# Performance work log

Measured on AMD Instinct MI355X. Metric: run time of the kernel, lower is better.

Reference implementation:

```python
import jax, jax.numpy as jnp
import numpy as np

COUPLE_STRENGTH = 0.1
ITER_FISTA = 16
ITER_EIGENVAL = 20


def setup_inputs() -> dict:
    key = jax.random.key(0)
    k1, k2 = jax.random.split(key)
    # light field patches: (b, N, u, v, s, t, ch)
    x = jax.random.normal(k1, (8, 256, 5, 5, 4, 4, 3), dtype=jnp.float32)
    dim_signal = 5 * 5 * 4 * 4 * 3  # 1200
    dim_dict = 2 * dim_signal       # overcompleteness = 2 -> 2400
    D = jax.random.normal(k2, (dim_signal, dim_dict), dtype=jnp.float32)
    D = D / jnp.linalg.norm(D, axis=0, keepdims=True)  # UnitNorm(axis=0) constraint
    return {"x": x, "dictionary": D}


def _max_eigval(D):
    """von Mises power iteration for largest eigenvalue of D^T D."""
    v0 = jax.random.normal(jax.random.key(42), (D.shape[1],), dtype=D.dtype)
    v0 = v0 / jnp.linalg.norm(v0)

    def step(v, _):
        w = D.T @ (D @ v)
        n = jnp.linalg.norm(w)
        return w / n, n

    _, norms = jax.lax.scan(step, v0, None, length=ITER_EIGENVAL)
    return norms[-1]


def _soft_threshold(x, thr):
    return jnp.sign(x) * jnp.maximum(jnp.abs(x) - thr, 0.0)


def _sparse_code_fista(x2, D):
    """x2: (B, N, dim_signal); D: (dim_signal, dim_dict) -> codes (B, N, dim_dict)."""
    L = _max_eigval(D)            # Lipschitz constant of grad of 0.5*||Dz - x||^2
    thr = COUPLE_STRENGTH / L
    z0 = jnp.zeros(x2.shape[:-1] + (D.shape[1],), dtype=x2.dtype)
    carry0 = (z0, z0, jnp.float32(1.0))  # (z, y, t)

    def step(carry, _):
        z, y, t = carry
        recon = jnp.einsum('bnk,dk->bnd', y, D)             # (B,N,ds)
        grad = jnp.einsum('bnd,dk->bnk', recon - x2, D)     # (B,N,dd)
        z_new = _soft_threshold(y - grad / L, thr)
        t_new = 0.5 * (1.0 + jnp.sqrt(1.0 + 4.0 * t * t))
        y_new = z_new + ((t - 1.0) / t_new) * (z_new - z)   # Nesterov momentum
        return (z_new, y_new, t_new), None

    (z, _, _), _ = jax.lax.scan(step, carry0, None, length=ITER_FISTA)
    return z


def reference(x, dictionary):
    B, N, u, v, s, t, ch = x.shape
    x2 = x.reshape(B, N, u * v * s * t * ch)
    code = jax.lax.stop_gradient(_sparse_code_fista(x2, dictionary))
    recon = jnp.einsum('bnk,dk->bnd', code, dictionary)  # matmul(x, D, transpose_b=True)
    return recon.reshape(B, N, u, v, s, t, ch)
```

## Files before the change

### kernel.cpp

```cpp
#include <hip/hip_runtime.h>
#include <hip/hip_bf16.h>
#include <cmath>

#define DS 1200
#define DD 2400
#define MR 2048
#define KP 1216
#define NP1 1280
#define NG 2432
#define PPI 150

typedef __attribute__((ext_vector_type(8))) short s16x8;
typedef __attribute__((ext_vector_type(4))) float f32x4;

__device__ __forceinline__ float s2f(short s) {
    union { unsigned u; float f; } c;
    c.u = ((unsigned)(unsigned short)s) << 16;
    return c.f;
}
__device__ __forceinline__ short f2s(float f) {
    __hip_bfloat16 h = __float2bfloat16(f);
    return *reinterpret_cast<short*>(&h);
}


__device__ __forceinline__ unsigned rotl32(unsigned x, int d) {
    return (x << d) | (x >> (32 - d));
}

__device__ void threefry2x32(unsigned k0, unsigned k1, unsigned x0, unsigned x1,
                             unsigned* o0, unsigned* o1) {
    unsigned ks0 = k0, ks1 = k1, ks2 = k0 ^ k1 ^ 0x1BD11BDAu;
    const int rotA[4] = {13, 15, 26, 6};
    const int rotB[4] = {17, 29, 16, 24};
    x0 += ks0; x1 += ks1;
    #pragma unroll
    for (int r = 0; r < 4; r++) { x0 += x1; x1 = rotl32(x1, rotA[r]); x1 ^= x0; }
    x0 += ks1; x1 += ks2 + 1u;
    #pragma unroll
    for (int r = 0; r < 4; r++) { x0 += x1; x1 = rotl32(x1, rotB[r]); x1 ^= x0; }
    x0 += ks2; x1 += ks0 + 2u;
    #pragma unroll
    for (int r = 0; r < 4; r++) { x0 += x1; x1 = rotl32(x1, rotA[r]); x1 ^= x0; }
    x0 += ks0; x1 += ks1 + 3u;
    #pragma unroll
    for (int r = 0; r < 4; r++) { x0 += x1; x1 = rotl32(x1, rotB[r]); x1 ^= x0; }
    x0 += ks1; x1 += ks2 + 4u;
    #pragma unroll
    for (int r = 0; r < 4; r++) { x0 += x1; x1 = rotl32(x1, rotA[r]); x1 ^= x0; }
    x0 += ks2; x1 += ks0 + 5u;
    *o0 = x0; *o1 = x1;
}

__device__ float erfinv_f32(float x) {
    float w = -logf((1.0f - x) * (1.0f + x));
    float p;
    if (w < 5.0f) {
        w -= 2.5f;
        p = 2.81022636e-08f;
        p = fmaf(p, w, 3.43273939e-07f);
        p = fmaf(p, w, -3.5233877e-06f);
        p = fmaf(p, w, -4.39150654e-06f);
        p = fmaf(p, w, 0.00021858087f);
        p = fmaf(p, w, -0.00125372503f);
        p = fmaf(p, w, -0.00417768164f);
        p = fmaf(p, w, 0.246640727f);
        p = fmaf(p, w, 1.50140941f);
    } else {
        w = sqrtf(w) - 3.0f;
        p = -0.000200214257f;
        p = fmaf(p, w, 0.000100950558f);
        p = fmaf(p, w, 0.00134934322f);
        p = fmaf(p, w, -0.00367342844f);
        p = fmaf(p, w, 0.00573950773f);
        p = fmaf(p, w, -0.0076224613f);
        p = fmaf(p, w, 0.00943887047f);
        p = fmaf(p, w, 1.00167406f);
        p = fmaf(p, w, 2.83297682f);
    }
    return p * x;
}

__device__ float bits_to_normal(unsigned bits) {
    unsigned fb = (bits >> 9) | 0x3F800000u;
    float u01 = __uint_as_float(fb) - 1.0f;
    const float lo = -0.99999994f;
    float u = u01 * 2.0f + lo;
    u = fmaxf(lo, u);
    return 1.41421356237f * erfinv_f32(u);
}

__global__ void k_init(float* __restrict__ w0, float* __restrict__ w1,
                       float* __restrict__ part) {
    int tid = threadIdx.x;
    for (int i = tid; i < 21 * PPI; i += 256) part[i] = 0.0f;
    if (tid < 32) {
        w0[2400 + tid] = 0.0f;
        w1[2400 + tid] = 0.0f;
    }
    __shared__ float red[256];
    float local2 = 0.0f;
    for (int p = tid; p < DS; p += 256) {
        unsigned r0, r1;
        threefry2x32(0u, 42u, (unsigned)p, (unsigned)(DS + p), &r0, &r1);
        float n0 = bits_to_normal(r0);
        float n1 = bits_to_normal(r1);
        w0[p] = n0;
        w0[DS + p] = n1;
        local2 += n0 * n0 + n1 * n1;
    }
    red[tid] = local2;
    __syncthreads();
    for (int s = 128; s > 0; s >>= 1) {
        if (tid < s) red[tid] += red[tid + s];
        __syncthreads();
    }
    if (tid == 0) part[0] = red[0];
}

__global__ __launch_bounds__(1024) void k_gmv(const short* __restrict__ Grm,
                                              const float* __restrict__ win,
                                              const float* __restrict__ partin,
                                              float* __restrict__ wout,
                                              float* __restrict__ partout) {
    float s2 = 0.0f;
    for (int i = 0; i < PPI; i++) s2 += partin[i];
    float rn = 1.0f / sqrtf(s2);
    int wave = threadIdx.x >> 6, lane = threadIdx.x & 63;
    int row = blockIdx.x * 16 + wave;
    const s16x8* gh = (const s16x8*)(Grm + (size_t)row * NG);
    const float4* w4 = (const float4*)win;
    float acc = 0.0f;
    #pragma unroll
    for (int i = 0; i < 5; i++) {
        int c = lane + i * 64;
        if (c < 304) {
            s16x8 h = gh[c];
            float4 wa = w4[c * 2], wb = w4[c * 2 + 1];
            acc += s2f(h[0]) * wa.x + s2f(h[1]) * wa.y;
            acc += s2f(h[2]) * wa.z + s2f(h[3]) * wa.w;
            acc += s2f(h[4]) * wb.x + s2f(h[5]) * wb.y;
            acc += s2f(h[6]) * wb.z + s2f(h[7]) * wb.w;
        }
    }
    #pragma unroll
    for (int off = 32; off > 0; off >>= 1) acc += __shfl_xor(acc, off, 64);
    __shared__ float red[16];
    if (lane == 0) {
        float val = acc * rn;
        wout[row] = val;
        red[wave] = val * val;
    }
    __syncthreads();
    if (threadIdx.x == 0) {
        float s = 0.0f;
        #pragma unroll
        for (int i = 0; i < 16; i++) s += red[i];
        partout[blockIdx.x] = s;
    }
}

__global__ void k_fin(const float* __restrict__ part20, float* __restrict__ scal) {
    if (threadIdx.x == 0) {
        float s = 0.0f;
        for (int i = 0; i < PPI; i++) s += part20[i];
        float L = sqrtf(s);
        scal[0] = L;
        scal[1] = 1.0f / L;
        scal[2] = 0.1f / L;
    }
}

__global__ void k_makeD(const float* __restrict__ D, short* __restrict__ Dp) {
    int p = blockIdx.x * 256 + threadIdx.x;
    if (p >= NP1 * NG) return;
    int tile = p >> 10, win = p & 1023;
    int row = win >> 3, e = win & 7;
    int mt = tile / (NG >> 3), ct = tile % (NG >> 3);
    int d = mt * 128 + row, n = ct * 8 + e;
    float v = (d < DS && n < DD) ? D[(size_t)d * DD + n] : 0.0f;
    Dp[p] = f2s(v);
}

__global__ void k_makeX(const float* __restrict__ x,
                        short* __restrict__ Xhi, short* __restrict__ Xlo) {
    int p = blockIdx.x * 256 + threadIdx.x;
    if (p >= MR * KP) return;
    int tile = p >> 10, win = p & 1023;
    int row = win >> 3, e = win & 7;
    int mt = tile / (KP >> 3), ct = tile % (KP >> 3);
    int m = mt * 128 + row, k = ct * 8 + e;
    float v = (k < DS) ? x[(size_t)m * DS + k] : 0.0f;
    short h = f2s(v);
    Xhi[p] = h;
    Xlo[p] = f2s(v - s2f(h));
}

__global__ void k_makeDt(const float* __restrict__ D,
                         short* __restrict__ Dthi, short* __restrict__ Dtlo) {
    __shared__ float t[32][33];
    int bc = blockIdx.x * 32;
    int bk = blockIdx.y * 32;
    int tx = threadIdx.x & 31, ty = threadIdx.x >> 5;
    for (int i = ty; i < 32; i += 8) {
        int k = bk + i, c = bc + tx;
        t[i][tx] = (k < DS && c < DD) ? D[(size_t)k * DD + c] : 0.0f;
    }
    __syncthreads();
    for (int i = ty; i < 32; i += 8) {
        int c = bc + i, k = bk + tx;
        float v = t[tx][i];
        short h = f2s(v);
        size_t po = ((size_t)(c >> 7) * (KP >> 3) + (k >> 3)) * 1024 +
                    ((c & 127) << 3) + (k & 7);
        Dthi[po] = h;
        Dtlo[po] = f2s(v - s2f(h));
    }
}

__global__ void k_makeW(const float* __restrict__ Gf, const float* __restrict__ scal,
                        short* __restrict__ Wp) {
    int i = blockIdx.x * 256 + threadIdx.x;
    if (i >= NG * NG / 8) return;
    float invL = scal[1];
    int e0 = i * 8;
    int band = e0 / (128 * NG);
    int rem = e0 - band * (128 * NG);
    int tile = rem >> 10;
    int row = (rem & 1023) >> 3;
    int m = band * 128 + row;
    int k0 = tile * 8;
    const float4* gp = (const float4*)(Gf + (size_t)m * NG + k0);
    float4 g0 = gp[0], g1 = gp[1];
    float gv[8] = {g0.x, g0.y, g0.z, g0.w, g1.x, g1.y, g1.z, g1.w};
    s16x8 wv;
    #pragma unroll
    for (int e = 0; e < 8; e++) {
        float wf = ((k0 + e == m) ? 1.0f : 0.0f) - gv[e] * invL;
        wv[e] = f2s(wf);
    }
    ((s16x8*)Wp)[i] = wv;
}

__global__ void k_fista0(const short* __restrict__ XDL, const float* __restrict__ scal,
                         short* __restrict__ Z, short* __restrict__ Y) {
    int i = blockIdx.x * 256 + threadIdx.x;
    if (i >= MR * NG / 8) return;
    float thr = scal[2];
    s16x8 xv = ((const s16x8*)XDL)[i];
    s16x8 zs;
    #pragma unroll
    for (int k = 0; k < 8; k++) {
        float gs = s2f(xv[k]);
        float az = fabsf(gs) - thr;
        float zn = (az > 0.0f) ? copysignf(az, gs) : 0.0f;
        zs[k] = f2s(zn);
    }
    ((s16x8*)Z)[i] = zs;
    ((s16x8*)Y)[i] = zs;
}

__device__ __forceinline__ void gload16(const void* g, void* l) {
    __builtin_amdgcn_global_load_lds(
        (const __attribute__((address_space(1))) unsigned int*)g,
        (__attribute__((address_space(3))) unsigned int*)l, 16, 0, 0);
}

template <int EPI, bool SPLIT>
__global__ __launch_bounds__(256, 2) void mfma_gemm(
    const short* __restrict__ Ah, const short* __restrict__ Al, int CA,
    const short* __restrict__ Bh, const short* __restrict__ Bl, int CB,
    int K, int swz,
    const short* __restrict__ XDLp, const float* __restrict__ scal, float mom,
    short* __restrict__ Ynew, short* __restrict__ Zst,
    short* __restrict__ Grm,
    float* __restrict__ Out) {
    constexpr int ALO = 2048;
    constexpr int BHO = 4096;
    constexpr int BLO = 8192;
    constexpr int BUF = 12288;
    __shared__ __align__(16) short lds[3 * BUF];

    const int tid = threadIdx.x;
    const int w = tid >> 6, lane = tid & 63;
    const int fm = lane & 15, kg = lane >> 4;
    const int wr = w >> 1, wc = w & 1;

    int bx, by;
    if (swz) {
        int q = gridDim.x >> 3;
        int s = (blockIdx.x & 7) * q + (blockIdx.x >> 3);
        by = s & 31; bx = s >> 5;
    } else { bx = blockIdx.x; by = blockIdx.y; }
    const int m0 = by * 64, n0 = bx * 128;

    f32x4 acc[2][4];
    #pragma unroll
    for (int g = 0; g < 2; ++g)
        #pragma unroll
        for (int h = 0; h < 4; ++h) acc[g][h] = f32x4{0.f, 0.f, 0.f, 0.f};

    float invL = 0.0f, thr = 0.0f;
    if (EPI == 2) thr = scal[2];
    if (EPI == 3) invL = scal[1];

    const int half = (m0 >> 6) & 1;
    const int nk = K / (SPLIT ? 32 : 64);

    const size_t AbS = (size_t)(m0 & ~127) * CA + w * 1024 + half * 512 + lane * 8;
    const size_t BbS = (size_t)n0 * CB + w * 512 + lane * 8;
    const size_t AbN = (size_t)(m0 & ~127) * CA + half * 512 + lane * 8;
    const size_t BbN = (size_t)n0 * CB + lane * 8;

    auto STAGE = [&](int t, int cur) {
        short* bp = &lds[cur * BUF];
        if constexpr (SPLIT) {
            const size_t kk = (size_t)t << 12;
            gload16(Ah + AbS + kk, bp + w * 512);
            gload16(Bh + BbS + kk, bp + BHO + w * 512);
            gload16(Bh + BbS + kk + 2048, bp + BHO + 2048 + w * 512);
            gload16(Al + AbS + kk, bp + ALO + w * 512);
            gload16(Bl + BbS + kk, bp + BLO + w * 512);
            gload16(Bl + BbS + kk + 2048, bp + BLO + 2048 + w * 512);
        } else {
            const size_t kk = (size_t)t << 13;
            const int cs0 = 2 * w, cs1 = 2 * w + 1;
            gload16(Ah + AbN + kk + cs0 * 1024, bp + cs0 * 512);
            gload16(Ah + AbN + kk + cs1 * 1024, bp + cs1 * 512);
            gload16(Bh + BbN + kk + cs0 * 1024,       bp + BHO + cs0 * 1024);
            gload16(Bh + BbN + kk + cs0 * 1024 + 512, bp + BHO + cs0 * 1024 + 512);
            gload16(Bh + BbN + kk + cs1 * 1024,       bp + BHO + cs1 * 1024);
            gload16(Bh + BbN + kk + cs1 * 1024 + 512, bp + BHO + cs1 * 1024 + 512);
        }
    };

    STAGE(0, 0);
    STAGE(1, 1);

    int rb = 0, sb = 2;
    for (int t = 0; t < nk; ++t) {
        if (t < nk - 1)
            asm volatile("s_waitcnt vmcnt(6)" ::: "memory");
        else
            asm volatile("s_waitcnt vmcnt(0)" ::: "memory");
        __builtin_amdgcn_s_barrier();
        asm volatile("" ::: "memory");
        if (t + 2 < nk) STAGE(t + 2, sb);
        const short* bs = &lds[rb * BUF];

        #pragma unroll
        for (int ks = 0; ks < (SPLIT ? 1 : 2); ++ks) {
            const int c = ks * 4 + kg;
            s16x8 a[2], b[4];
            #pragma unroll
            for (int g = 0; g < 2; ++g)
                a[g] = *(const s16x8*)&bs[c * 512 + (wr * 32 + g * 16 + fm) * 8];
            #pragma unroll
            for (int h = 0; h < 4; ++h)
                b[h] = *(const s16x8*)&bs[BHO + c * 1024 + (wc * 64 + h * 16 + fm) * 8];
            if constexpr (SPLIT) {
                s16x8 a2[2], b2[4];
                #pragma unroll
                for (int g = 0; g < 2; ++g)
                    a2[g] = *(const s16x8*)&bs[ALO + c * 512 + (wr * 32 + g * 16 + fm) * 8];
                #pragma unroll
                for (int h = 0; h < 4; ++h)
                    b2[h] = *(const s16x8*)&bs[BLO + c * 1024 + (wc * 64 + h * 16 + fm) * 8];
                #pragma unroll
                for (int g = 0; g < 2; ++g)
                    #pragma unroll
                    for (int h = 0; h < 4; ++h) {
                        acc[g][h] = __builtin_amdgcn_mfma_f32_16x16x32_bf16(a[g], b[h], acc[g][h], 0, 0, 0);
                        acc[g][h] = __builtin_amdgcn_mfma_f32_16x16x32_bf16(a[g], b2[h], acc[g][h], 0, 0, 0);
                        acc[g][h] = __builtin_amdgcn_mfma_f32_16x16x32_bf16(a2[g], b[h], acc[g][h], 0, 0, 0);
                    }
            } else {
                #pragma unroll
                for (int g = 0; g < 2; ++g)
                    #pragma unroll
                    for (int h = 0; h < 4; ++h)
                        acc[g][h] = __builtin_amdgcn_mfma_f32_16x16x32_bf16(a[g], b[h], acc[g][h], 0, 0, 0);
            }
        }
        rb = (rb == 2) ? 0 : rb + 1;
        sb = (sb == 2) ? 0 : sb + 1;
    }

    #pragma unroll
    for (int g = 0; g < 2; ++g) {
        #pragma unroll
        for (int h = 0; h < 4; ++h) {
            #pragma unroll
            for (int j = 0; j < 4; ++j) {
                int m = m0 + wr * 32 + g * 16 + kg * 4 + j;
                int n = n0 + wc * 64 + h * 16 + fm;
                float v = acc[g][h][j];
                if (EPI == 0) {
                    if (n < DS) Out[(size_t)m * DS + n] = v;
                } else if (EPI == 2) {
                    size_t pz = (size_t)(m & ~127) * NG + ((n >> 3) << 10) +
                                ((m & 127) << 3) + (n & 7);
                    float gs = v + s2f(XDLp[pz]);
                    float az = fabsf(gs) - thr;
                    float zn = (az > 0.0f) ? copysignf(az, gs) : 0.0f;
                    float zold = s2f(Zst[pz]);
                    float yn = zn + mom * (zn - zold);
                    Zst[pz] = f2s(zn);
                    Ynew[pz] = f2s(yn);
                } else if (EPI == 3) {
                    size_t pz = (size_t)(m & ~127) * NG + ((n >> 3) << 10) +
                                ((m & 127) << 3) + (n & 7);
                    Ynew[pz] = f2s(v * invL);
                } else {
                    size_t o = (size_t)m * NG + n;
                    Grm[o] = f2s(v);
                    Out[o] = v;
                }
            }
        }
    }
}

extern "C" void kernel_launch(void* const* d_in, const int* in_sizes, int n_in,
                              void* d_out, int out_size, void* d_ws, size_t ws_size,
                              hipStream_t stream) {
    const float* x = (const float*)d_in[0];
    const float* D = (const float*)d_in[1];
    float* out = (float*)d_out;

    char* wsb = (char*)d_ws;
    float* w0 = (float*)wsb;
    float* w1 = w0 + 2432;
    float* part = w1 + 2432;
    float* scal = part + 3200;

    char* p = wsb + 65536;
    short* Dp   = (short*)p; p += (size_t)NP1 * NG * 2;
    short* Dthi = (short*)p; p += (size_t)NG * KP * 2;
    short* Dtlo = (short*)p; p += (size_t)NG * KP * 2;
    short* Xhi  = (short*)p; p += (size_t)MR * KP * 2;
    short* Xlo  = (short*)p; p += (size_t)MR * KP * 2;
    short* Wp   = (short*)p; p += (size_t)NG * NG * 2;
    short* Grm  = (short*)p; p += (size_t)NG * NG * 2;
    short* XDLp = (short*)p; p += (size_t)MR * NG * 2;
    short* Ya   = (short*)p; p += (size_t)MR * NG * 2;
    short* Yb   = (short*)p; p += (size_t)MR * NG * 2;
    short* Zp   = (short*)p; p += (size_t)MR * NG * 2;
    float* Gf   = (float*)Ya;

    k_makeD<<<(NP1 * NG + 255) / 256, 256, 0, stream>>>(D, Dp);
    k_makeDt<<<dim3(NG / 32, KP / 32), 256, 0, stream>>>(D, Dthi, Dtlo);
    k_makeX<<<(MR * KP + 255) / 256, 256, 0, stream>>>(x, Xhi, Xlo);

    mfma_gemm<4, true><<<dim3(NG / 128, NG / 64), 256, 0, stream>>>(
        Dthi, Dtlo, KP, Dthi, Dtlo, KP, KP, 0,
        nullptr, nullptr, 0.0f, nullptr, nullptr, Grm, Gf);

    k_init<<<1, 256, 0, stream>>>(w0, w1, part);
    for (int j = 0; j < 20; j++) {
        const float* win = (j & 1) ? w1 : w0;
        float* wout = (j & 1) ? w0 : w1;
        k_gmv<<<PPI, 1024, 0, stream>>>(Grm, win, part + j * PPI, wout,
                                        part + (j + 1) * PPI);
    }
    k_fin<<<1, 64, 0, stream>>>(part + 20 * PPI, scal);

    k_makeW<<<(NG * NG / 8 + 255) / 256, 256, 0, stream>>>(Gf, scal, Wp);

    mfma_gemm<3, true><<<dim3(608), 256, 0, stream>>>(
        Xhi, Xlo, KP, Dthi, Dtlo, KP, KP, 1,
        nullptr, scal, 0.0f, XDLp, nullptr, nullptr, nullptr);

    k_fista0<<<(MR * NG / 8 + 255) / 256, 256, 0, stream>>>(XDLp, scal, Zp, Ya);

    float t = 1.6180339887f;
    for (int i = 1; i < 16; i++) {
        float tn = 0.5f * (1.0f + sqrtf(1.0f + 4.0f * t * t));
        float mom = (t - 1.0f) / tn;
        t = tn;
        short* Yc = (i & 1) ? Ya : Yb;
        short* Yn = (i & 1) ? Yb : Ya;
        mfma_gemm<2, false><<<dim3(608), 256, 0, stream>>>(
            Yc, nullptr, NG, Wp, nullptr, NG, NG, 1,
            XDLp, scal, mom, Yn, Zp, nullptr, nullptr);
    }

    mfma_gemm<0, false><<<dim3(320), 256, 0, stream>>>(
        Zp, nullptr, NG, Dp, nullptr, NG, NG, 1,
        nullptr, nullptr, 0.0f, nullptr, nullptr, nullptr, out);
}
```

Measured before the change: 1.002 ms.

## Fuse power iteration into cooperative kernel, shrink GEMM pipeline for occupancy

Replaces the 20 per-iteration matvec launches plus the finalize kernel with a single cooperative kernel that loops over iterations using grid-wide syncs. It stops writing the fp32 Gram copy, so makeW reads the bf16 Gram, which lowers precision of W slightly. The GEMM goes from a three-buffer LDS pipeline with manual waitcnt to two buffers with __syncthreads, and launch bounds are raised to 4 blocks per CU to increase occupancy. The risk is less latency hiding in the GEMM's main loop, plus grid.sync overhead.

```diff
diff --git a/kernel.cpp b/kernel.cpp
--- a/kernel.cpp
+++ b/kernel.cpp
@@ -1,6 +1,9 @@
 #include <hip/hip_runtime.h>
 #include <hip/hip_bf16.h>
+#include <hip/hip_cooperative_groups.h>
 #include <cmath>
+
+namespace cg = cooperative_groups;
 
 #define DS 1200
 #define DD 2400
@@ -8,7 +11,7 @@
 #define KP 1216
 #define NP1 1280
 #define NG 2432
-#define PPI 150
+#define PB 152
 
 typedef __attribute__((ext_vector_type(8))) short s16x8;
 typedef __attribute__((ext_vector_type(4))) float f32x4;
@@ -93,7 +96,7 @@
 __global__ void k_init(float* __restrict__ w0, float* __restrict__ w1,
                        float* __restrict__ part) {
     int tid = threadIdx.x;
-    for (int i = tid; i < 21 * PPI; i += 256) part[i] = 0.0f;
+    for (int i = tid; i < 21 * PB; i += 256) part[i] = 0.0f;
     if (tid < 32) {
         w0[2400 + tid] = 0.0f;
         w1[2400 + tid] = 0.0f;
@@ -118,52 +121,62 @@
     if (tid == 0) part[0] = red[0];
 }
 
-__global__ __launch_bounds__(1024) void k_gmv(const short* __restrict__ Grm,
-                                              const float* __restrict__ win,
-                                              const float* __restrict__ partin,
-                                              float* __restrict__ wout,
-                                              float* __restrict__ partout) {
-    float s2 = 0.0f;
-    for (int i = 0; i < PPI; i++) s2 += partin[i];
-    float rn = 1.0f / sqrtf(s2);
-    int wave = threadIdx.x >> 6, lane = threadIdx.x & 63;
-    int row = blockIdx.x * 16 + wave;
+__global__ __launch_bounds__(1024) void k_power(const short* __restrict__ Grm,
+                                                float* __restrict__ w0,
+                                                float* __restrict__ w1,
+                                                float* __restrict__ part,
+                                                float* __restrict__ scal) {
+    cg::grid_group grid = cg::this_grid();
+    const int wv = threadIdx.x >> 6, lane = threadIdx.x & 63;
+    const int row = blockIdx.x * 16 + wv;
+    __shared__ float red[16];
+    __shared__ float rns;
+
     const s16x8* gh = (const s16x8*)(Grm + (size_t)row * NG);
-    const float4* w4 = (const float4*)win;
-    float acc = 0.0f;
-    #pragma unroll
-    for (int i = 0; i < 5; i++) {
-        int c = lane + i * 64;
-        if (c < 304) {
-            s16x8 h = gh[c];
-            float4 wa = w4[c * 2], wb = w4[c * 2 + 1];
-            acc += s2f(h[0]) * wa.x + s2f(h[1]) * wa.y;
-            acc += s2f(h[2]) * wa.z + s2f(h[3]) * wa.w;
-            acc += s2f(h[4]) * wb.x + s2f(h[5]) * wb.y;
-            acc += s2f(h[6]) * wb.z + s2f(h[7]) * wb.w;
-        }
-    }
-    #pragma unroll
-    for (int off = 32; off > 0; off >>= 1) acc += __shfl_xor(acc, off, 64);
-    __shared__ float red[16];
-    if (lane == 0) {
-        float val = acc * rn;
-        wout[row] = val;
-        red[wave] = val * val;
-    }
-    __syncthreads();
-    if (threadIdx.x == 0) {
+
+    for (int j = 0; j < 20; ++j) {
+        const float* win = (j & 1) ? w1 : w0;
+        float* wout = (j & 1) ? w0 : w1;
+        if (threadIdx.x == 0) {
+            float s = 0.0f;
+            for (int b = 0; b < PB; ++b) s += part[j * PB + b];
+            rns = 1.0f / sqrtf(s);
+        }
+        __syncthreads();
+        const float rn = rns;
+        const float4* w4 = (const float4*)win;
+        float acc = 0.0f;
+        #pragma unroll
+        for (int i = 0; i < 5; i++) {
+            int c = lane + i * 64;
+            if (c < 304) {
+                s16x8 h = gh[c];
+                float4 wa = w4[c * 2], wb = w4[c * 2 + 1];
+                acc += s2f(h[0]) * wa.x + s2f(h[1]) * wa.y;
+                acc += s2f(h[2]) * wa.z + s2f(h[3]) * wa.w;
+                acc += s2f(h[4]) * wb.x + s2f(h[5]) * wb.y;
+                acc += s2f(h[6]) * wb.z + s2f(h[7]) * wb.w;
+            }
+        }
+        #pragma unroll
+        for (int off = 32; off > 0; off >>= 1) acc += __shfl_xor(acc, off, 64);
+        if (lane == 0) {
+            float val = acc * rn;
+            wout[row] = val;
+            red[wv] = val * val;
+        }
+        __syncthreads();
+        if (threadIdx.x == 0) {
+            float s = 0.0f;
+            #pragma unroll
+            for (int i = 0; i < 16; i++) s += red[i];
+            part[(j + 1) * PB + blockIdx.x] = s;
+        }
+        grid.sync();
+    }
+    if (blockIdx.x == 0 && threadIdx.x == 0) {
         float s = 0.0f;
-        #pragma unroll
-        for (int i = 0; i < 16; i++) s += red[i];
-        partout[blockIdx.x] = s;
-    }
-}
-
-__global__ void k_fin(const float* __restrict__ part20, float* __restrict__ scal) {
-    if (threadIdx.x == 0) {
-        float s = 0.0f;
-        for (int i = 0; i < PPI; i++) s += part20[i];
+        for (int b = 0; b < PB; ++b) s += part[20 * PB + b];
         float L = sqrtf(s);
         scal[0] = L;
         scal[1] = 1.0f / L;
@@ -218,7 +231,7 @@
     }
 }
 
-__global__ void k_makeW(const float* __restrict__ Gf, const float* __restrict__ scal,
+__global__ void k_makeW(const short* __restrict__ Grm, const float* __restrict__ scal,
                         short* __restrict__ Wp) {
     int i = blockIdx.x * 256 + threadIdx.x;
     if (i >= NG * NG / 8) return;
@@ -230,13 +243,11 @@
     int row = (rem & 1023) >> 3;
     int m = band * 128 + row;
     int k0 = tile * 8;
-    const float4* gp = (const float4*)(Gf + (size_t)m * NG + k0);
-    float4 g0 = gp[0], g1 = gp[1];
-    float gv[8] = {g0.x, g0.y, g0.z, g0.w, g1.x, g1.y, g1.z, g1.w};
+    s16x8 g = *(const s16x8*)(Grm + (size_t)m * NG + k0);
     s16x8 wv;
     #pragma unroll
     for (int e = 0; e < 8; e++) {
-        float wf = ((k0 + e == m) ? 1.0f : 0.0f) - gv[e] * invL;
+        float wf = ((k0 + e == m) ? 1.0f : 0.0f) - s2f(g[e]) * invL;
         wv[e] = f2s(wf);
     }
     ((s16x8*)Wp)[i] = wv;
@@ -267,7 +278,7 @@
 }
 
 template <int EPI, bool SPLIT>
-__global__ __launch_bounds__(256, 2) void mfma_gemm(
+__global__ __launch_bounds__(256, 4) void mfma_gemm(
     const short* __restrict__ Ah, const short* __restrict__ Al, int CA,
     const short* __restrict__ Bh, const short* __restrict__ Bl, int CB,
     int K, int swz,
@@ -279,7 +290,7 @@
     constexpr int BHO = 4096;
     constexpr int BLO = 8192;
     constexpr int BUF = 12288;
-    __shared__ __align__(16) short lds[3 * BUF];
+    __shared__ __align__(16) short lds[2 * BUF];
 
     const int tid = threadIdx.x;
     const int w = tid >> 6, lane = tid & 63;
@@ -335,18 +346,11 @@
     };
 
     STAGE(0, 0);
-    STAGE(1, 1);
-
-    int rb = 0, sb = 2;
+
     for (int t = 0; t < nk; ++t) {
-        if (t < nk - 1)
-            asm volatile("s_waitcnt vmcnt(6)" ::: "memory");
-        else
-            asm volatile("s_waitcnt vmcnt(0)" ::: "memory");
-        __builtin_amdgcn_s_barrier();
-        asm volatile("" ::: "memory");
-        if (t + 2 < nk) STAGE(t + 2, sb);
-        const short* bs = &lds[rb * BUF];
+        __syncthreads();
+        if (t + 1 < nk) STAGE(t + 1, (t + 1) & 1);
+        const short* bs = &lds[(t & 1) * BUF];
 
         #pragma unroll
         for (int ks = 0; ks < (SPLIT ? 1 : 2); ++ks) {
@@ -382,8 +386,6 @@
                         acc[g][h] = __builtin_amdgcn_mfma_f32_16x16x32_bf16(a[g], b[h], acc[g][h], 0, 0, 0);
             }
         }
-        rb = (rb == 2) ? 0 : rb + 1;
-        sb = (sb == 2) ? 0 : sb + 1;
     }
 
     #pragma unroll
@@ -412,9 +414,7 @@
                                 ((m & 127) << 3) + (n & 7);
                     Ynew[pz] = f2s(v * invL);
                 } else {
-                    size_t o = (size_t)m * NG + n;
-                    Grm[o] = f2s(v);
-                    Out[o] = v;
+                    Grm[(size_t)m * NG + n] = f2s(v);
                 }
             }
         }
@@ -446,7 +446,6 @@
     short* Ya   = (short*)p; p += (size_t)MR * NG * 2;
     short* Yb   = (short*)p; p += (size_t)MR * NG * 2;
     short* Zp   = (short*)p; p += (size_t)MR * NG * 2;
-    float* Gf   = (float*)Ya;
 
     k_makeD<<<(NP1 * NG + 255) / 256, 256, 0, stream>>>(D, Dp);
     k_makeDt<<<dim3(NG / 32, KP / 32), 256, 0, stream>>>(D, Dthi, Dtlo);
@@ -454,18 +453,17 @@
 
     mfma_gemm<4, true><<<dim3(NG / 128, NG / 64), 256, 0, stream>>>(
         Dthi, Dtlo, KP, Dthi, Dtlo, KP, KP, 0,
-        nullptr, nullptr, 0.0f, nullptr, nullptr, Grm, Gf);
+        nullptr, nullptr, 0.0f, nullptr, nullptr, Grm, nullptr);
 
     k_init<<<1, 256, 0, stream>>>(w0, w1, part);
-    for (int j = 0; j < 20; j++) {
-        const float* win = (j & 1) ? w1 : w0;
-        float* wout = (j & 1) ? w0 : w1;
-        k_gmv<<<PPI, 1024, 0, stream>>>(Grm, win, part + j * PPI, wout,
-                                        part + (j + 1) * PPI);
-    }
-    k_fin<<<1, 64, 0, stream>>>(part + 20 * PPI, scal);
-
-    k_makeW<<<(NG * NG / 8 + 255) / 256, 256, 0, stream>>>(Gf, scal, Wp);
+    {
+        void* kargs[] = {(void*)&Grm, (void*)&w0, (void*)&w1,
+                         (void*)&part, (void*)&scal};
+        hipLaunchCooperativeKernel((void*)k_power, dim3(PB), dim3(1024),
+                                   kargs, 0, stream);
+    }
+
+    k_makeW<<<(NG * NG / 8 + 255) / 256, 256, 0, stream>>>(Grm, scal, Wp);
 
     mfma_gemm<3, true><<<dim3(608), 256, 0, stream>>>(
         Xhi, Xlo, KP, Dthi, Dtlo, KP, KP, 1,
```

After: 1.185 ms. 18.2% more time.

## Double-buffer GEMM for higher occupancy, drop X low split, specialize last FISTA step

Applied to the files above, without the earlier changes.

The GEMM pipeline shrinks from a triple-buffered LDS ring with vmcnt waits to double buffering with __syncthreads, and launch bounds rise to four blocks per SM to gain occupancy. The X·D GEMM drops the X low-part split (new SPLITM=2 mode, two MFMAs instead of three). The fp32 Gram output is removed, so W is built from the bf16 Gram. The final FISTA iteration uses a new epilogue that writes only Z and skips the Y update. These changes reduce memory traffic and MFMA work but lower precision and shorten the prefetch distance.

```diff
diff --git a/kernel.cpp b/kernel.cpp
--- a/kernel.cpp
+++ b/kernel.cpp
@@ -182,8 +182,7 @@
     Dp[p] = f2s(v);
 }
 
-__global__ void k_makeX(const float* __restrict__ x,
-                        short* __restrict__ Xhi, short* __restrict__ Xlo) {
+__global__ void k_makeX(const float* __restrict__ x, short* __restrict__ Xp) {
     int p = blockIdx.x * 256 + threadIdx.x;
     if (p >= MR * KP) return;
     int tile = p >> 10, win = p & 1023;
@@ -191,9 +190,7 @@
     int mt = tile / (KP >> 3), ct = tile % (KP >> 3);
     int m = mt * 128 + row, k = ct * 8 + e;
     float v = (k < DS) ? x[(size_t)m * DS + k] : 0.0f;
-    short h = f2s(v);
-    Xhi[p] = h;
-    Xlo[p] = f2s(v - s2f(h));
+    Xp[p] = f2s(v);
 }
 
 __global__ void k_makeDt(const float* __restrict__ D,
@@ -218,7 +215,7 @@
     }
 }
 
-__global__ void k_makeW(const float* __restrict__ Gf, const float* __restrict__ scal,
+__global__ void k_makeW(const short* __restrict__ Grm, const float* __restrict__ scal,
                         short* __restrict__ Wp) {
     int i = blockIdx.x * 256 + threadIdx.x;
     if (i >= NG * NG / 8) return;
@@ -230,13 +227,11 @@
     int row = (rem & 1023) >> 3;
     int m = band * 128 + row;
     int k0 = tile * 8;
-    const float4* gp = (const float4*)(Gf + (size_t)m * NG + k0);
-    float4 g0 = gp[0], g1 = gp[1];
-    float gv[8] = {g0.x, g0.y, g0.z, g0.w, g1.x, g1.y, g1.z, g1.w};
+    s16x8 g = *(const s16x8*)(Grm + (size_t)m * NG + k0);
     s16x8 wv;
     #pragma unroll
     for (int e = 0; e < 8; e++) {
-        float wf = ((k0 + e == m) ? 1.0f : 0.0f) - gv[e] * invL;
+        float wf = ((k0 + e == m) ? 1.0f : 0.0f) - s2f(g[e]) * invL;
         wv[e] = f2s(wf);
     }
     ((s16x8*)Wp)[i] = wv;
@@ -266,8 +261,8 @@
         (__attribute__((address_space(3))) unsigned int*)l, 16, 0, 0);
 }
 
-template <int EPI, bool SPLIT>
-__global__ __launch_bounds__(256, 2) void mfma_gemm(
+template <int EPI, int SPLITM>
+__global__ __launch_bounds__(256, 4) void mfma_gemm(
     const short* __restrict__ Ah, const short* __restrict__ Al, int CA,
     const short* __restrict__ Bh, const short* __restrict__ Bl, int CB,
     int K, int swz,
@@ -279,7 +274,7 @@
     constexpr int BHO = 4096;
     constexpr int BLO = 8192;
     constexpr int BUF = 12288;
-    __shared__ __align__(16) short lds[3 * BUF];
+    __shared__ __align__(16) short lds[2 * BUF];
 
     const int tid = threadIdx.x;
     const int w = tid >> 6, lane = tid & 63;
@@ -301,11 +296,11 @@
         for (int h = 0; h < 4; ++h) acc[g][h] = f32x4{0.f, 0.f, 0.f, 0.f};
 
     float invL = 0.0f, thr = 0.0f;
-    if (EPI == 2) thr = scal[2];
+    if (EPI == 2 || EPI == 5) thr = scal[2];
     if (EPI == 3) invL = scal[1];
 
     const int half = (m0 >> 6) & 1;
-    const int nk = K / (SPLIT ? 32 : 64);
+    const int nk = K / (SPLITM ? 32 : 64);
 
     const size_t AbS = (size_t)(m0 & ~127) * CA + w * 1024 + half * 512 + lane * 8;
     const size_t BbS = (size_t)n0 * CB + w * 512 + lane * 8;
@@ -314,12 +309,19 @@
 
     auto STAGE = [&](int t, int cur) {
         short* bp = &lds[cur * BUF];
-        if constexpr (SPLIT) {
+        if constexpr (SPLITM == 1) {
             const size_t kk = (size_t)t << 12;
             gload16(Ah + AbS + kk, bp + w * 512);
             gload16(Bh + BbS + kk, bp + BHO + w * 512);
             gload16(Bh + BbS + kk + 2048, bp + BHO + 2048 + w * 512);
             gload16(Al + AbS + kk, bp + ALO + w * 512);
+            gload16(Bl + BbS + kk, bp + BLO + w * 512);
+            gload16(Bl + BbS + kk + 2048, bp + BLO + 2048 + w * 512);
+        } else if constexpr (SPLITM == 2) {
+            const size_t kk = (size_t)t << 12;
+            gload16(Ah + AbS + kk, bp + w * 512);
+            gload16(Bh + BbS + kk, bp + BHO + w * 512);
+            gload16(Bh + BbS + kk + 2048, bp + BHO + 2048 + w * 512);
             gload16(Bl + BbS + kk, bp + BLO + w * 512);
             gload16(Bl + BbS + kk + 2048, bp + BLO + 2048 + w * 512);
         } else {
@@ -335,21 +337,14 @@
     };
 
     STAGE(0, 0);
-    STAGE(1, 1);
-
-    int rb = 0, sb = 2;
+
     for (int t = 0; t < nk; ++t) {
-        if (t < nk - 1)
-            asm volatile("s_waitcnt vmcnt(6)" ::: "memory");
-        else
-            asm volatile("s_waitcnt vmcnt(0)" ::: "memory");
-        __builtin_amdgcn_s_barrier();
-        asm volatile("" ::: "memory");
-        if (t + 2 < nk) STAGE(t + 2, sb);
-        const short* bs = &lds[rb * BUF];
+        __syncthreads();
+        if (t + 1 < nk) STAGE(t + 1, (t + 1) & 1);
+        const short* bs = &lds[(t & 1) * BUF];
 
         #pragma unroll
-        for (int ks = 0; ks < (SPLIT ? 1 : 2); ++ks) {
+        for (int ks = 0; ks < (SPLITM ? 1 : 2); ++ks) {
             const int c = ks * 4 + kg;
             s16x8 a[2], b[4];
             #pragma unroll
@@ -358,7 +353,7 @@
             #pragma unroll
             for (int h = 0; h < 4; ++h)
                 b[h] = *(const s16x8*)&bs[BHO + c * 1024 + (wc * 64 + h * 16 + fm) * 8];
-            if constexpr (SPLIT) {
+            if constexpr (SPLITM == 1) {
                 s16x8 a2[2], b2[4];
                 #pragma unroll
                 for (int g = 0; g < 2; ++g)
@@ -374,6 +369,18 @@
                         acc[g][h] = __builtin_amdgcn_mfma_f32_16x16x32_bf16(a[g], b2[h], acc[g][h], 0, 0, 0);
                         acc[g][h] = __builtin_amdgcn_mfma_f32_16x16x32_bf16(a2[g], b[h], acc[g][h], 0, 0, 0);
                     }
+            } else if constexpr (SPLITM == 2) {
+                s16x8 b2[4];
+                #pragma unroll
+                for (int h = 0; h < 4; ++h)
+                    b2[h] = *(const s16x8*)&bs[BLO + c * 1024 + (wc * 64 + h * 16 + fm) * 8];
+                #pragma unroll
+                for (int g = 0; g < 2; ++g)
+                    #pragma unroll
+                    for (int h = 0; h < 4; ++h) {
+                        acc[g][h] = __builtin_amdgcn_mfma_f32_16x16x32_bf16(a[g], b[h], acc[g][h], 0, 0, 0);
+                        acc[g][h] = __builtin_amdgcn_mfma_f32_16x16x32_bf16(a[g], b2[h], acc[g][h], 0, 0, 0);
+                    }
             } else {
                 #pragma unroll
                 for (int g = 0; g < 2; ++g)
@@ -382,8 +389,6 @@
                         acc[g][h] = __builtin_amdgcn_mfma_f32_16x16x32_bf16(a[g], b[h], acc[g][h], 0, 0, 0);
             }
         }
-        rb = (rb == 2) ? 0 : rb + 1;
-        sb = (sb == 2) ? 0 : sb + 1;
     }
 
     #pragma unroll
@@ -407,14 +412,19 @@
                     float yn = zn + mom * (zn - zold);
                     Zst[pz] = f2s(zn);
                     Ynew[pz] = f2s(yn);
+                } else if (EPI == 5) {
+                    size_t pz = (size_t)(m & ~127) * NG + ((n >> 3) << 10) +
+                                ((m & 127) << 3) + (n & 7);
+                    float gs = v + s2f(XDLp[pz]);
+                    float az = fabsf(gs) - thr;
+                    float zn = (az > 0.0f) ? copysignf(az, gs) : 0.0f;
+                    Zst[pz] = f2s(zn);
                 } else if (EPI == 3) {
                     size_t pz = (size_t)(m & ~127) * NG + ((n >> 3) << 10) +
                                 ((m & 127) << 3) + (n & 7);
                     Ynew[pz] = f2s(v * invL);
                 } else {
-                    size_t o = (size_t)m * NG + n;
-                    Grm[o] = f2s(v);
-                    Out[o] = v;
+                    Grm[(size_t)m * NG + n] = f2s(v);
                 }
             }
         }
@@ -438,23 +448,21 @@
     short* Dp   = (short*)p; p += (size_t)NP1 * NG * 2;
     short* Dthi = (short*)p; p += (size_t)NG * KP * 2;
     short* Dtlo = (short*)p; p += (size_t)NG * KP * 2;
-    short* Xhi  = (short*)p; p += (size_t)MR * KP * 2;
-    short* Xlo  = (short*)p; p += (size_t)MR * KP * 2;
+    short* Xp   = (short*)p; p += (size_t)MR * KP * 2;
     short* Wp   = (short*)p; p += (size_t)NG * NG * 2;
     short* Grm  = (short*)p; p += (size_t)NG * NG * 2;
     short* XDLp = (short*)p; p += (size_t)MR * NG * 2;
     short* Ya   = (short*)p; p += (size_t)MR * NG * 2;
     short* Yb   = (short*)p; p += (size_t)MR * NG * 2;
     short* Zp   = (short*)p; p += (size_t)MR * NG * 2;
-    float* Gf   = (float*)Ya;
 
     k_makeD<<<(NP1 * NG + 255) / 256, 256, 0, stream>>>(D, Dp);
     k_makeDt<<<dim3(NG / 32, KP / 32), 256, 0, stream>>>(D, Dthi, Dtlo);
-    k_makeX<<<(MR * KP + 255) / 256, 256, 0, stream>>>(x, Xhi, Xlo);
-
-    mfma_gemm<4, true><<<dim3(NG / 128, NG / 64), 256, 0, stream>>>(
+    k_makeX<<<(MR * KP + 255) / 256, 256, 0, stream>>>(x, Xp);
+
+    mfma_gemm<4, 1><<<dim3(NG / 128, NG / 64), 256, 0, stream>>>(
         Dthi, Dtlo, KP, Dthi, Dtlo, KP, KP, 0,
-        nullptr, nullptr, 0.0f, nullptr, nullptr, Grm, Gf);
+        nullptr, nullptr, 0.0f, nullptr, nullptr, Grm, nullptr);
 
     k_init<<<1, 256, 0, stream>>>(w0, w1, part);
     for (int j = 0; j < 20; j++) {
@@ -465,27 +473,33 @@
     }
     k_fin<<<1, 64, 0, stream>>>(part + 20 * PPI, scal);
 
-    k_makeW<<<(NG * NG / 8 + 255) / 256, 256, 0, stream>>>(Gf, scal, Wp);
-
-    mfma_gemm<3, true><<<dim3(608), 256, 0, stream>>>(
-        Xhi, Xlo, KP, Dthi, Dtlo, KP, KP, 1,
+    k_makeW<<<(NG * NG / 8 + 255) / 256, 256, 0, stream>>>(Grm, scal, Wp);
+
+    mfma_gemm<3, 2><<<dim3(608), 256, 0, stream>>>(
+        Xp, nullptr, KP, Dthi, Dtlo, KP, KP, 1,
         nullptr, scal, 0.0f, XDLp, nullptr, nullptr, nullptr);
 
     k_fista0<<<(MR * NG / 8 + 255) / 256, 256, 0, stream>>>(XDLp, scal, Zp, Ya);
 
     float t = 1.6180339887f;
-    for (int i = 1; i < 16; i++) {
+    for (int i = 1; i < 15; i++) {
         float tn = 0.5f * (1.0f + sqrtf(1.0f + 4.0f * t * t));
         float mom = (t - 1.0f) / tn;
         t = tn;
         short* Yc = (i & 1) ? Ya : Yb;
         short* Yn = (i & 1) ? Yb : Ya;
-        mfma_gemm<2, false><<<dim3(608), 256, 0, stream>>>(
+        mfma_gemm<2, 0><<<dim3(608), 256, 0, stream>>>(
             Yc, nullptr, NG, Wp, nullptr, NG, NG, 1,
             XDLp, scal, mom, Yn, Zp, nullptr, nullptr);
     }
-
-    mfma_gemm<0, false><<<dim3(320), 256, 0, stream>>>(
+    {
+        short* Yc = Ya;
+        mfma_gemm<5, 0><<<dim3(608), 256, 0, stream>>>(
+            Yc, nullptr, NG, Wp, nullptr, NG, NG, 1,
+            XDLp, scal, 0.0f, nullptr, Zp, nullptr, nullptr);
+    }
+
+    mfma_gemm<0, 0><<<dim3(320), 256, 0, stream>>>(
         Zp, nullptr, NG, Dp, nullptr, NG, NG, 1,
         nullptr, nullptr, 0.0f, nullptr, nullptr, nullptr, out);
 }
```

Measured after the change: 857.7 us (median of 2 runs). -14.4%, faster.
